# Kernel optimization log

Hardware: AMD Instinct MI355X
Metric: run time of the kernel (lower is better)

## Reference

```python
import jax, jax.numpy as jnp
import numpy as np

EPS_RMS = 1e-6
EPS_SCALE = 1e-5


def setup_inputs() -> dict:
    key = jax.random.key(0)
    k1, k2 = jax.random.split(key)
    B, S, D_IN, D_OUT = 4, 2048, 2048, 8192
    x = jax.random.normal(k1, (B, S, D_IN), dtype=jnp.float32)
    # kaiming_uniform-ish init bound
    bound = 1.0 / np.sqrt(D_IN)
    weight = jax.random.uniform(k2, (D_OUT, D_IN), dtype=jnp.float32, minval=-bound, maxval=bound)
    gamma = jnp.ones((D_IN,), dtype=jnp.float32)
    return {"x": x, "weight": weight, "gamma": gamma}


def rmsnorm(x, gamma):
    xf = x.astype(jnp.float32)
    inv = jax.lax.rsqrt(jnp.mean(xf * xf, axis=-1, keepdims=True) + EPS_RMS)
    return (xf * inv).astype(x.dtype) * gamma


def quantize_weights_ternary(weight):
    scale = jnp.maximum(jnp.mean(jnp.abs(weight)), EPS_SCALE)
    wn = weight / scale
    wq = jax.lax.stop_gradient(jnp.round(jnp.clip(wn, -1.0, 1.0)) - wn) + wn  # STE
    return wq, scale


def reference(x, weight, gamma):
    x_norm = rmsnorm(x, gamma)                      # [B, S, D_in]
    wq, scale = quantize_weights_ternary(weight)    # [D_out, D_in], scalar
    out = jnp.einsum('bsd,od->bso', x_norm, wq)     # [B, S, D_out]
    return out * scale
```

## Files before the change

### kernel.cpp

```cpp
#include <hip/hip_runtime.h>
#include <hip/hip_bf16.h>
#include <stdint.h>

#define M_ROWS 8192
#define K_DIM  2048
#define N_DIM  8192
#define W_ELEMS (N_DIM * K_DIM)
#define X_ELEMS (M_ROWS * K_DIM)
#define NT 32
#define ABSUM_BLOCKS 256

typedef __bf16 v8bf __attribute__((ext_vector_type(8)));
typedef float  v4f  __attribute__((ext_vector_type(4)));

__device__ inline unsigned short f2bf(float f) {
  uint32_t u = __builtin_bit_cast(uint32_t, f);
  uint32_t r = (u + 0x7fffu + ((u >> 16) & 1u)) >> 16;
  return (unsigned short)r;
}

__device__ inline void async_copy16(const void* g, void* l) {
  __builtin_amdgcn_global_load_lds(
      (const __attribute__((address_space(1))) void*)g,
      (__attribute__((address_space(3))) void*)l, 16, 0, 0);
}

__global__ __launch_bounds__(256) void prep_kernel(const float* __restrict__ X,
                                                   const float* __restrict__ gamma,
                                                   const float* __restrict__ W,
                                                   unsigned short* __restrict__ Xn,
                                                   double* __restrict__ partials) {
  __shared__ double wsumd[4];
  __shared__ float wsumf[4];
  const int t = threadIdx.x;
  const int lane = t & 63, wid = t >> 6;

  if (blockIdx.x < ABSUM_BLOCKS) {
    const int pb = blockIdx.x;
    int tid = pb * 256 + t;
    const float4* W4 = (const float4*)W;
    const int n4 = W_ELEMS / 4;
    double acc = 0.0;
    for (int i = tid; i < n4; i += ABSUM_BLOCKS * 256) {
      float4 v = W4[i];
      acc += (double)fabsf(v.x) + (double)fabsf(v.y) +
             (double)fabsf(v.z) + (double)fabsf(v.w);
    }
    for (int off = 32; off > 0; off >>= 1) acc += __shfl_down(acc, off);
    if (lane == 0) wsumd[wid] = acc;
    __syncthreads();
    if (t == 0) partials[pb] = wsumd[0] + wsumd[1] + wsumd[2] + wsumd[3];
    return;
  }

  const int row = blockIdx.x - ABSUM_BLOCKS;
  const float4* xr = (const float4*)(X + (size_t)row * K_DIM);
  float4 a = xr[t * 2];
  float4 b = xr[t * 2 + 1];
  float ss = a.x * a.x + a.y * a.y + a.z * a.z + a.w * a.w +
             b.x * b.x + b.y * b.y + b.z * b.z + b.w * b.w;
  for (int off = 32; off > 0; off >>= 1) ss += __shfl_down(ss, off);
  if (lane == 0) wsumf[wid] = ss;
  __syncthreads();
  float total = wsumf[0] + wsumf[1] + wsumf[2] + wsumf[3];
  float inv = 1.0f / sqrtf(total * (1.0f / (float)K_DIM) + 1e-6f);
  const float4* gr = (const float4*)gamma;
  float4 g0 = gr[t * 2];
  float4 g1 = gr[t * 2 + 1];
  union { unsigned short h[8]; uint4 u; } p;
  p.h[0] = f2bf((a.x * inv) * g0.x);
  p.h[1] = f2bf((a.y * inv) * g0.y);
  p.h[2] = f2bf((a.z * inv) * g0.z);
  p.h[3] = f2bf((a.w * inv) * g0.w);
  p.h[4] = f2bf((b.x * inv) * g1.x);
  p.h[5] = f2bf((b.y * inv) * g1.y);
  p.h[6] = f2bf((b.z * inv) * g1.z);
  p.h[7] = f2bf((b.w * inv) * g1.w);
  ((uint4*)(Xn + (size_t)row * K_DIM))[t] = p.u;
}

__global__ __launch_bounds__(256) void reduce_kernel(const double* __restrict__ partials,
                                                     float* __restrict__ scale) {
  double v = partials[threadIdx.x];
  for (int off = 32; off > 0; off >>= 1) v += __shfl_down(v, off);
  __shared__ double ws[4];
  int lane = threadIdx.x & 63, wid = threadIdx.x >> 6;
  if (lane == 0) ws[wid] = v;
  __syncthreads();
  if (threadIdx.x == 0) {
    double total = ws[0] + ws[1] + ws[2] + ws[3];
    scale[0] = (float)fmax(total * (1.0 / (double)W_ELEMS), 1e-5);
  }
}

__global__ __launch_bounds__(256) void quant_kernel(const float* __restrict__ W,
                                                    const float* __restrict__ scale,
                                                    unsigned short* __restrict__ Wq) {
  float s = scale[0];
  size_t idx = ((size_t)blockIdx.x * 256 + threadIdx.x) * 8;
  const float4* w4 = (const float4*)(W + idx);
  float4 a = w4[0];
  float4 b = w4[1];
  union { unsigned short h[8]; uint4 u; } p;
  p.h[0] = f2bf(rintf(fminf(1.f, fmaxf(-1.f, a.x / s))));
  p.h[1] = f2bf(rintf(fminf(1.f, fmaxf(-1.f, a.y / s))));
  p.h[2] = f2bf(rintf(fminf(1.f, fmaxf(-1.f, a.z / s))));
  p.h[3] = f2bf(rintf(fminf(1.f, fmaxf(-1.f, a.w / s))));
  p.h[4] = f2bf(rintf(fminf(1.f, fmaxf(-1.f, b.x / s))));
  p.h[5] = f2bf(rintf(fminf(1.f, fmaxf(-1.f, b.y / s))));
  p.h[6] = f2bf(rintf(fminf(1.f, fmaxf(-1.f, b.z / s))));
  p.h[7] = f2bf(rintf(fminf(1.f, fmaxf(-1.f, b.w / s))));
  *(uint4*)(Wq + idx) = p.u;
}

__global__ __launch_bounds__(512, 2) void gemm_kernel(
    const unsigned short* __restrict__ A,
    const unsigned short* __restrict__ B,
    const float* __restrict__ scale,
    float* __restrict__ C) {
  __shared__ __align__(16) char lds[131072];

  const int tid = threadIdx.x;
  const int lane = tid & 63;
  const int wave = tid >> 6;
  const int wm = wave & 1;
  const int wn = wave >> 1;

  const int bid = blockIdx.x;
  const int swz = (bid & 7) * 128 + (bid >> 3);
  const int st = swz >> 4, wi = swz & 15;
  const int mb = (st >> 3) * 4 + (wi >> 2);
  const int nb = (st & 7) * 4 + (wi & 3);
  const int m0 = mb * 256;
  const int n0 = nb * 256;

  const int srow3 = lane >> 3;
  const int scg = (lane & 7) ^ srow3;

  const int aoff_a = wm * 8192 + (lane & 15) * 128;
  const int boff_b = wn * 4096 + (lane & 15) * 128;
  const int swzk0 = ((lane >> 4) ^ (lane & 7)) << 4;
  const int swzk1 = ((4 + (lane >> 4)) ^ (lane & 7)) << 4;

  v4f acc[8][4] = {};
  v8bf af[4][2];
  v8bf b0f[2][2];
  v8bf b1f[2][2];

#define STAGE_A(B_, H_, KT_) do {                                              \
    _Pragma("unroll")                                                          \
    for (int j = 0; j < 2; ++j) {                                              \
      const int chunk_ = wave * 2 + j;                                         \
      const int slot_ = chunk_ * 8 + srow3;                                    \
      const int row_ = ((slot_ >> 6) << 7) + ((H_) << 6) + (slot_ & 63);       \
      async_copy16(A + (size_t)(m0 + row_) * K_DIM + ((KT_) << 6) + (scg << 3),\
                   lds + (B_) * 32768 + (H_) * 16384 + chunk_ * 1024);         \
    } } while (0)

#define STAGE_B(B_, H_, KT_) do {                                              \
    _Pragma("unroll")                                                          \
    for (int j = 0; j < 2; ++j) {                                              \
      const int chunk_ = wave * 2 + j;                                         \
      const int slot_ = chunk_ * 8 + srow3;                                    \
      const int row_ = ((slot_ >> 5) << 6) + ((H_) << 5) + (slot_ & 31);       \
      async_copy16(B + (size_t)(n0 + row_) * K_DIM + ((KT_) << 6) + (scg << 3),\
                   lds + 65536 + (B_) * 32768 + (H_) * 16384 + chunk_ * 1024); \
    } } while (0)

#define LOADA(B_, QM_) do {                                                    \
    _Pragma("unroll")                                                          \
    for (int tm = 0; tm < 4; ++tm) {                                           \
      af[tm][0] = *(const v8bf*)(lds + (B_) * 32768 + (QM_) * 16384 +          \
                                 aoff_a + tm * 2048 + swzk0);                  \
      af[tm][1] = *(const v8bf*)(lds + (B_) * 32768 + (QM_) * 16384 +          \
                                 aoff_a + tm * 2048 + swzk1);                  \
    } } while (0)

#define LOADB(B_, QN_, DST) do {                                               \
    _Pragma("unroll")                                                          \
    for (int tn = 0; tn < 2; ++tn) {                                           \
      DST[tn][0] = *(const v8bf*)(lds + 65536 + (B_) * 32768 + (QN_) * 16384 + \
                                  boff_b + tn * 2048 + swzk0);                 \
      DST[tn][1] = *(const v8bf*)(lds + 65536 + (B_) * 32768 + (QN_) * 16384 + \
                                  boff_b + tn * 2048 + swzk1);                 \
    } } while (0)

#define MMAC(BF, QM_, QN_) do {                                                \
    _Pragma("unroll")                                                          \
    for (int ks = 0; ks < 2; ++ks)                                             \
    _Pragma("unroll")                                                          \
    for (int tm = 0; tm < 4; ++tm)                                             \
    _Pragma("unroll")                                                          \
    for (int tn = 0; tn < 2; ++tn)                                             \
      acc[(QM_) * 4 + tm][(QN_) * 2 + tn] =                                    \
          __builtin_amdgcn_mfma_f32_16x16x32_bf16(                             \
              BF[tn][ks], af[tm][ks],                                          \
              acc[(QM_) * 4 + tm][(QN_) * 2 + tn], 0, 0, 0);                   \
  } while (0)

#define BARRIER() __builtin_amdgcn_s_barrier()
#define VM8() asm volatile("s_waitcnt vmcnt(8)" ::: "memory")

#define TILE(T_, B_) do {                                                      \
    const int t1_ = ((T_) + 1 < NT) ? (T_) + 1 : NT - 1;                       \
    const int t2_ = ((T_) + 2 < NT) ? (T_) + 2 : NT - 1;                       \
               \
    LOADA(B_, 0);                                                              \
    STAGE_A(1 - (B_), 1, t1_);                                                 \
    BARRIER();                                                                 \
    __builtin_amdgcn_s_setprio(1); MMAC(b0f, 0, 0);                            \
    __builtin_amdgcn_s_setprio(0);                                             \
    BARRIER();                                                                 \
                                                            \
    LOADB(B_, 1, b1f);                                                         \
    BARRIER();                                                                 \
    __builtin_amdgcn_s_setprio(1); MMAC(b1f, 0, 1);                            \
    __builtin_amdgcn_s_setprio(0);                                             \
    VM8(); BARRIER();                                                          \
                                                            \
    LOADA(B_, 1);                                                              \
    STAGE_A(B_, 0, t2_);                                                       \
    STAGE_B(B_, 1, t2_);                                                       \
    BARRIER();                                                                 \
    __builtin_amdgcn_s_setprio(1); MMAC(b0f, 1, 0);                            \
    __builtin_amdgcn_s_setprio(0);                                             \
    BARRIER();                                                                 \
                  \
    STAGE_B(B_, 0, t2_);                                                       \
    VM8(); BARRIER();                                                          \
    LOADB(1 - (B_), 0, b0f);                                                   \
    __builtin_amdgcn_s_setprio(1); MMAC(b1f, 1, 1);                            \
    __builtin_amdgcn_s_setprio(0);                                             \
    BARRIER();                                                                 \
  } while (0)

  STAGE_A(0, 0, 0);
  STAGE_B(0, 0, 0);
  STAGE_B(0, 1, 0);
  STAGE_A(0, 1, 0);
  STAGE_A(1, 0, 1);
  STAGE_B(1, 1, 1);
  STAGE_B(1, 0, 1);
  VM8();
  BARRIER();
  LOADB(0, 0, b0f);

  for (int t = 0; t < NT; t += 2) {
    TILE(t, 0);
    TILE(t + 1, 1);
  }

  const float s = scale[0];
  const int mBase = m0 + wm * 128 + (lane & 15);
  const int nBase = n0 + wn * 64 + ((lane >> 4) << 2);
#pragma unroll
  for (int tm = 0; tm < 8; ++tm) {
#pragma unroll
    for (int tn = 0; tn < 4; ++tn) {
      float4 v;
      v.x = acc[tm][tn][0] * s;
      v.y = acc[tm][tn][1] * s;
      v.z = acc[tm][tn][2] * s;
      v.w = acc[tm][tn][3] * s;
      *(float4*)&C[(size_t)(mBase + tm * 16) * N_DIM + (nBase + tn * 16)] = v;
    }
  }

#undef STAGE_A
#undef STAGE_B
#undef LOADA
#undef LOADB
#undef MMAC
#undef BARRIER
#undef VM8
#undef TILE
}

extern "C" void kernel_launch(void* const* d_in, const int* in_sizes, int n_in,
                              void* d_out, int out_size, void* d_ws, size_t ws_size,
                              hipStream_t stream) {
  const float* x = (const float*)d_in[0];
  const float* w = (const float*)d_in[1];
  const float* gamma = (const float*)d_in[2];
  float* out = (float*)d_out;

  float* scale_f = (float*)d_ws;
  unsigned short* xn = (unsigned short*)((char*)d_ws + 16);
  unsigned short* wq = (unsigned short*)((char*)d_ws + 16 + (size_t)X_ELEMS * 2);
  double* partials = (double*)wq;

  prep_kernel<<<ABSUM_BLOCKS + M_ROWS, 256, 0, stream>>>(x, gamma, w, xn, partials);
  reduce_kernel<<<1, 256, 0, stream>>>(partials, scale_f);
  quant_kernel<<<W_ELEMS / (256 * 8), 256, 0, stream>>>(w, scale_f, wq);
  gemm_kernel<<<(M_ROWS / 256) * (N_DIM / 256), 512, 0, stream>>>(xn, wq, scale_f, out);
}
```

Baseline: 611.5 us.

## Coalesce prep/quant accesses, remap GEMM tiles per XCD, nontemporal output stores

The prep and quant kernels now have each thread read two float4s a block-stride apart instead of two adjacent ones, so wavefront loads and stores are contiguous. The GEMM block-to-tile mapping is redone so each XCD works on a band of M rows and a spread of N columns, aiming for better L2 reuse of A and B tiles. Output stores become nontemporal so the large fp32 result does not pollute cache. Trade-offs: each thread now issues narrower 8-byte stores in the prep kernels, and the new tile mapping could lower reuse if it does not match the hardware's dispatch order.

```diff
diff --git a/kernel.cpp b/kernel.cpp
--- a/kernel.cpp
+++ b/kernel.cpp
@@ -55,8 +55,8 @@
 
   const int row = blockIdx.x - ABSUM_BLOCKS;
   const float4* xr = (const float4*)(X + (size_t)row * K_DIM);
-  float4 a = xr[t * 2];
-  float4 b = xr[t * 2 + 1];
+  float4 a = xr[t];
+  float4 b = xr[t + 256];
   float ss = a.x * a.x + a.y * a.y + a.z * a.z + a.w * a.w +
              b.x * b.x + b.y * b.y + b.z * b.z + b.w * b.w;
   for (int off = 32; off > 0; off >>= 1) ss += __shfl_down(ss, off);
@@ -65,18 +65,20 @@
   float total = wsumf[0] + wsumf[1] + wsumf[2] + wsumf[3];
   float inv = 1.0f / sqrtf(total * (1.0f / (float)K_DIM) + 1e-6f);
   const float4* gr = (const float4*)gamma;
-  float4 g0 = gr[t * 2];
-  float4 g1 = gr[t * 2 + 1];
-  union { unsigned short h[8]; uint4 u; } p;
-  p.h[0] = f2bf((a.x * inv) * g0.x);
-  p.h[1] = f2bf((a.y * inv) * g0.y);
-  p.h[2] = f2bf((a.z * inv) * g0.z);
-  p.h[3] = f2bf((a.w * inv) * g0.w);
-  p.h[4] = f2bf((b.x * inv) * g1.x);
-  p.h[5] = f2bf((b.y * inv) * g1.y);
-  p.h[6] = f2bf((b.z * inv) * g1.z);
-  p.h[7] = f2bf((b.w * inv) * g1.w);
-  ((uint4*)(Xn + (size_t)row * K_DIM))[t] = p.u;
+  float4 g0 = gr[t];
+  float4 g1 = gr[t + 256];
+  union { unsigned short h[4]; uint2 u; } pa, pb;
+  pa.h[0] = f2bf((a.x * inv) * g0.x);
+  pa.h[1] = f2bf((a.y * inv) * g0.y);
+  pa.h[2] = f2bf((a.z * inv) * g0.z);
+  pa.h[3] = f2bf((a.w * inv) * g0.w);
+  pb.h[0] = f2bf((b.x * inv) * g1.x);
+  pb.h[1] = f2bf((b.y * inv) * g1.y);
+  pb.h[2] = f2bf((b.z * inv) * g1.z);
+  pb.h[3] = f2bf((b.w * inv) * g1.w);
+  uint2* orow = (uint2*)(Xn + (size_t)row * K_DIM);
+  orow[t] = pa.u;
+  orow[t + 256] = pb.u;
 }
 
 __global__ __launch_bounds__(256) void reduce_kernel(const double* __restrict__ partials,
@@ -97,20 +99,22 @@
                                                     const float* __restrict__ scale,
                                                     unsigned short* __restrict__ Wq) {
   float s = scale[0];
-  size_t idx = ((size_t)blockIdx.x * 256 + threadIdx.x) * 8;
-  const float4* w4 = (const float4*)(W + idx);
-  float4 a = w4[0];
-  float4 b = w4[1];
-  union { unsigned short h[8]; uint4 u; } p;
-  p.h[0] = f2bf(rintf(fminf(1.f, fmaxf(-1.f, a.x / s))));
-  p.h[1] = f2bf(rintf(fminf(1.f, fmaxf(-1.f, a.y / s))));
-  p.h[2] = f2bf(rintf(fminf(1.f, fmaxf(-1.f, a.z / s))));
-  p.h[3] = f2bf(rintf(fminf(1.f, fmaxf(-1.f, a.w / s))));
-  p.h[4] = f2bf(rintf(fminf(1.f, fmaxf(-1.f, b.x / s))));
-  p.h[5] = f2bf(rintf(fminf(1.f, fmaxf(-1.f, b.y / s))));
-  p.h[6] = f2bf(rintf(fminf(1.f, fmaxf(-1.f, b.z / s))));
-  p.h[7] = f2bf(rintf(fminf(1.f, fmaxf(-1.f, b.w / s))));
-  *(uint4*)(Wq + idx) = p.u;
+  const int t = threadIdx.x;
+  const float4* W4 = (const float4*)W + (size_t)blockIdx.x * 512;
+  float4 a = W4[t];
+  float4 b = W4[t + 256];
+  union { unsigned short h[4]; uint2 u; } pa, pb;
+  pa.h[0] = f2bf(rintf(fminf(1.f, fmaxf(-1.f, a.x / s))));
+  pa.h[1] = f2bf(rintf(fminf(1.f, fmaxf(-1.f, a.y / s))));
+  pa.h[2] = f2bf(rintf(fminf(1.f, fmaxf(-1.f, a.z / s))));
+  pa.h[3] = f2bf(rintf(fminf(1.f, fmaxf(-1.f, a.w / s))));
+  pb.h[0] = f2bf(rintf(fminf(1.f, fmaxf(-1.f, b.x / s))));
+  pb.h[1] = f2bf(rintf(fminf(1.f, fmaxf(-1.f, b.y / s))));
+  pb.h[2] = f2bf(rintf(fminf(1.f, fmaxf(-1.f, b.z / s))));
+  pb.h[3] = f2bf(rintf(fminf(1.f, fmaxf(-1.f, b.w / s))));
+  uint2* o = (uint2*)(Wq + (size_t)blockIdx.x * 2048);
+  o[t] = pa.u;
+  o[t + 256] = pb.u;
 }
 
 __global__ __launch_bounds__(512, 2) void gemm_kernel(
@@ -127,10 +131,12 @@
   const int wn = wave >> 1;
 
   const int bid = blockIdx.x;
-  const int swz = (bid & 7) * 128 + (bid >> 3);
-  const int st = swz >> 4, wi = swz & 15;
-  const int mb = (st >> 3) * 4 + (wi >> 2);
-  const int nb = (st & 7) * 4 + (wi & 3);
+  const int xcd = bid & 7;
+  const int idx = bid >> 3;
+  const int half = idx >> 6;
+  const int i6 = idx & 63;
+  const int mb = xcd * 2 + half * 16 + ((i6 >> 2) & 1);
+  const int nb = (i6 >> 3) * 4 + (i6 & 3);
   const int m0 = mb * 256;
   const int n0 = nb * 256;
 
@@ -225,7 +231,7 @@
     __builtin_amdgcn_s_setprio(1); MMAC(b0f, 1, 0);                            \
     __builtin_amdgcn_s_setprio(0);                                             \
     BARRIER();                                                                 \
-                  \
+                             \
     STAGE_B(B_, 0, t2_);                                                       \
     VM8(); BARRIER();                                                          \
     LOADB(1 - (B_), 0, b0f);                                                   \
@@ -257,12 +263,9 @@
   for (int tm = 0; tm < 8; ++tm) {
 #pragma unroll
     for (int tn = 0; tn < 4; ++tn) {
-      float4 v;
-      v.x = acc[tm][tn][0] * s;
-      v.y = acc[tm][tn][1] * s;
-      v.z = acc[tm][tn][2] * s;
-      v.w = acc[tm][tn][3] * s;
-      *(float4*)&C[(size_t)(mBase + tm * 16) * N_DIM + (nBase + tn * 16)] = v;
+      v4f v = acc[tm][tn] * s;
+      __builtin_nontemporal_store(
+          v, (v4f*)&C[(size_t)(mBase + tm * 16) * N_DIM + (nBase + tn * 16)]);
     }
   }
 
@@ -291,6 +294,6 @@
 
   prep_kernel<<<ABSUM_BLOCKS + M_ROWS, 256, 0, stream>>>(x, gamma, w, xn, partials);
   reduce_kernel<<<1, 256, 0, stream>>>(partials, scale_f);
-  quant_kernel<<<W_ELEMS / (256 * 8), 256, 0, stream>>>(w, scale_f, wq);
+  quant_kernel<<<W_ELEMS / 2048, 256, 0, stream>>>(w, scale_f, wq);
   gemm_kernel<<<(M_ROWS / 256) * (N_DIM / 256), 512, 0, stream>>>(xn, wq, scale_f, out);
 }
```

Measured after the change: 605.6 us. No clear change (-1.0%).
